# Kernel optimization log

Hardware: AMD Instinct MI355X
Metric: run time of the kernel (lower is better)

The kernel has to match this reference:

```python
import jax, jax.numpy as jnp
import numpy as np

IN_COUNT = 1024
OUT_COUNT = 1024
NUM_BASIS = 8
INPUT_ABS_MAX = 1.0
X_MIN = 0.0
X_MAX = 1.0
GAMMA_SCALE = 3.0
BATCH = 4096


def setup_inputs() -> dict:
    key = jax.random.key(0)
    k_x, k_c = jax.random.split(key)
    x = jax.random.normal(k_x, (BATCH, IN_COUNT), dtype=jnp.float32)
    coeffs = 0.01 * jax.random.normal(k_c, (OUT_COUNT, IN_COUNT, NUM_BASIS), dtype=jnp.float32)
    # fixed buffers
    centers_1d = jnp.linspace(X_MIN, X_MAX, NUM_BASIS)
    centers = jnp.broadcast_to(centers_1d[None, :], (IN_COUNT, NUM_BASIS)).astype(jnp.float32)
    delta = (X_MAX - X_MIN) / (NUM_BASIS - 1)
    gamma = GAMMA_SCALE / delta
    slopes = jnp.full((IN_COUNT, NUM_BASIS), gamma, dtype=jnp.float32)
    alpha = jnp.full((IN_COUNT,), (X_MAX - X_MIN) / (2.0 * INPUT_ABS_MAX), dtype=jnp.float32)
    beta = jnp.full((IN_COUNT,), 0.5 * (X_MIN + X_MAX), dtype=jnp.float32)
    return {"x": x, "coeffs": coeffs, "centers": centers, "slopes": slopes, "alpha": alpha, "beta": beta}


def reference(x, coeffs, centers, slopes, alpha, beta):
    # u: (B, in) affine transform with fixed alpha/beta
    u = alpha[None, :] * x + beta[None, :]
    # basis: (B, in, basis) = 0.5*(1+tanh(slope*(u - center)))
    basis = 0.5 * (1.0 + jnp.tanh(slopes[None, :, :] * (u[:, :, None] - centers[None, :, :])))
    # y[b,o] = sum_{i,m} coeffs[o,i,m] * basis[b,i,m]  (fused GEMM over in*basis)
    y = jnp.einsum('bim,oim->bo', basis, coeffs)
    return y
```

## Files before the change

kernel.cpp:

```cpp
#include <hip/hip_runtime.h>
#include <hip/hip_bf16.h>
#include <cstdint>
#include <cstddef>

#define BATCH 4096
#define INC   1024
#define OUTC  1024
#define NB    8
#define KDIM  (INC * NB)

#define BM 256
#define BN 256
#define BKB 64
#define SPLITS 4
#define KZ (KDIM / SPLITS)
#define KSTEPS (KZ / BKB)
#define GRID_BLOCKS ((OUTC / BN) * (BATCH / BM) * SPLITS)

#define EXPAND_BLOCKS  ((BATCH * INC) / 256)
#define QUANT_BLOCKS   OUTC
#define PREP_BLOCKS    (EXPAND_BLOCKS + QUANT_BLOCKS)

typedef int   v4i __attribute__((ext_vector_type(4)));
typedef char  v8c __attribute__((ext_vector_type(8)));
typedef short v8s __attribute__((ext_vector_type(8)));

__device__ __forceinline__ unsigned short f2bf(float f) {
  union { float f; unsigned u; } v; v.f = f;
  unsigned r = v.u + 0x7fffu + ((v.u >> 16) & 1u);
  return (unsigned short)(r >> 16);
}
__device__ __forceinline__ float bf2f(unsigned short h) {
  union { unsigned u; float f; } v; v.u = ((unsigned)h) << 16; return v.f;
}

__device__ __forceinline__ void gld16(const char* g, char* l) {
  __builtin_amdgcn_global_load_lds(
      (const __attribute__((address_space(1))) unsigned int*)g,
      (__attribute__((address_space(3))) unsigned int*)l, 16, 0, 0);
}

__global__ __launch_bounds__(256) void prep_kernel(
    const float* __restrict__ x, const float4* __restrict__ coeffs4,
    const float* __restrict__ centers, const float* __restrict__ slopes,
    const float* __restrict__ alpha, const float* __restrict__ beta,
    char* __restrict__ Ai8, int* __restrict__ Ci8i,
    float* __restrict__ maxrow, int* __restrict__ qcsum) {
  const int blk = blockIdx.x;
  const int tid = threadIdx.x;
  if (blk < EXPAND_BLOCKS) {
    const int idx = blk * 256 + tid;
    const int i = idx & (INC - 1);
    const float u = alpha[i] * x[idx] + beta[i];
    const float s0 = slopes[i * NB];
    const float c0 = centers[i * NB];
    const float c1 = centers[i * NB + 1];
    const float L2E2 = 2.8853900817779268f;
    const float a2 = L2E2 * s0;
    float e = __builtin_amdgcn_exp2f(a2 * (c0 - u));
    const float R = __builtin_amdgcn_exp2f(a2 * (c1 - c0));
    v8c q;
#pragma unroll
    for (int m = 0; m < 8; ++m) {
      float basis = __builtin_amdgcn_rcpf(1.0f + e);
      q[m] = (char)(int)rintf(basis * 254.0f - 127.0f);
      e *= R;
    }
    *(v8c*)(Ai8 + (size_t)idx * 8) = q;
  } else {
    const int o = blk - EXPAND_BLOCKS;
    const float4* row = coeffs4 + (size_t)o * (KDIM / 4);
    float4 v[8];
    float m = 0.0f;
#pragma unroll
    for (int j = 0; j < 8; ++j) {
      v[j] = row[tid + 256 * j];
      m = fmaxf(m, fmaxf(fmaxf(fabsf(v[j].x), fabsf(v[j].y)),
                         fmaxf(fabsf(v[j].z), fabsf(v[j].w))));
    }
#pragma unroll
    for (int off = 32; off; off >>= 1) m = fmaxf(m, __shfl_xor(m, off));
    __shared__ float wm[4];
    __shared__ int   wq[4];
    if ((tid & 63) == 0) wm[tid >> 6] = m;
    __syncthreads();
    const float M = fmaxf(fmaxf(fmaxf(wm[0], wm[1]), fmaxf(wm[2], wm[3])), 1e-30f);
    const float s = 127.0f / M;
    int qs = 0;
#pragma unroll
    for (int j = 0; j < 8; ++j) {
      int q0 = (int)rintf(v[j].x * s), q1 = (int)rintf(v[j].y * s);
      int q2 = (int)rintf(v[j].z * s), q3 = (int)rintf(v[j].w * s);
      Ci8i[(size_t)o * (KDIM / 4) + tid + 256 * j] =
          (q0 & 0xFF) | ((q1 & 0xFF) << 8) | ((q2 & 0xFF) << 16) | ((q3 & 0xFF) << 24);
      qs += q0 + q1 + q2 + q3;
    }
#pragma unroll
    for (int off = 32; off; off >>= 1) qs += __shfl_xor(qs, off);
    if ((tid & 63) == 0) wq[tid >> 6] = qs;
    __syncthreads();
    if (tid == 0) { maxrow[o] = M; qcsum[o] = wq[0] + wq[1] + wq[2] + wq[3]; }
  }
}

__global__ __launch_bounds__(512, 2) void gemm_kernel(
    const char* __restrict__ A, const char* __restrict__ C,
    unsigned short* __restrict__ partials) {
  __shared__ __align__(16) char As[3][BM * BKB];
  __shared__ __align__(16) char Bs[3][BN * BKB];

  const int id = (blockIdx.x & 7) * (GRID_BLOCKS / 8) + (blockIdx.x >> 3);
  const int z  = id >> 6;
  const int p  = id & 63;
  const int by = p >> 2;
  const int bx = p & 3;
  const int bm0 = by * BM;
  const int bn0 = bx * BN;
  const int kt0 = z * KZ;

  const int tid  = threadIdx.x;
  const int wave = tid >> 6;
  const int lane = tid & 63;
  const int quad = lane >> 4;
  const int lm   = lane & 15;
  const int wm   = (wave >> 2) * 128;
  const int wn   = (wave & 3) * 64;

  const int r4 = lane >> 2;
  const int gg = (lane & 3) ^ ((lane >> 3) & 3);

  const char* pA0 = A + (size_t)(bm0 + wave * 32 + r4) * KDIM + kt0 + gg * 16;
  const char* pB0 = C + (size_t)(bn0 + wave * 32 + r4) * KDIM + kt0 + gg * 16;
  const int lo = wave * 32 * BKB;

  v4i acc[8][4] = {};
  const int kx = (quad ^ ((lm >> 1) & 3)) * 16;

  static_assert(KSTEPS >= 3 && (KSTEPS - 2) % 1 == 0, "pipeline needs >=3 steps");

#define STAGE(SL)                                                            \
  {                                                                          \
    _Pragma("unroll")                                                        \
    for (int j = 0; j < 2; ++j) {                                            \
      gld16(pA0 + (size_t)j * (16 * KDIM), As[SL] + lo + j * (16 * BKB));    \
      gld16(pB0 + (size_t)j * (16 * KDIM), Bs[SL] + lo + j * (16 * BKB));    \
    }                                                                        \
    pA0 += BKB; pB0 += BKB;                                                  \
  }

#define STEP(SL, VMSTR, DOSTAGE)                                             \
  {                                                                          \
    asm volatile("s_waitcnt vmcnt(" VMSTR ")" ::: "memory");                 \
    __builtin_amdgcn_sched_barrier(0);                                       \
    __builtin_amdgcn_s_barrier();                                            \
    const char* cA = As[SL];                                                 \
    const char* cB = Bs[SL];                                                 \
    v4i a[4], b[4], a2[4];                                                   \
    _Pragma("unroll")                                                        \
    for (int f = 0; f < 4; ++f)                                              \
      a[f] = *(const v4i*)(cA + (wm + f * 16 + lm) * BKB + kx);              \
    _Pragma("unroll")                                                        \
    for (int f = 0; f < 4; ++f)                                              \
      b[f] = *(const v4i*)(cB + (wn + f * 16 + lm) * BKB + kx);              \
    _Pragma("unroll")                                                        \
    for (int f = 0; f < 4; ++f)                                              \
      a2[f] = *(const v4i*)(cA + (wm + (f + 4) * 16 + lm) * BKB + kx);       \
    asm volatile("s_waitcnt lgkmcnt(4)" ::: "memory");                       \
    __builtin_amdgcn_sched_barrier(0);                                       \
    __builtin_amdgcn_s_setprio(1);                                           \
    _Pragma("unroll")                                                        \
    for (int fm = 0; fm < 4; ++fm)                                           \
      _Pragma("unroll")                                                      \
      for (int fn = 0; fn < 4; ++fn)                                         \
        acc[fm][fn] = __builtin_amdgcn_mfma_i32_16x16x64_i8(a[fm], b[fn], acc[fm][fn], 0, 0, 0); \
    __builtin_amdgcn_s_setprio(0);                                           \
    asm volatile("s_waitcnt lgkmcnt(0)" ::: "memory");                       \
    __builtin_amdgcn_sched_barrier(0);                                       \
    __builtin_amdgcn_s_setprio(1);                                           \
    _Pragma("unroll")                                                        \
    for (int fm = 0; fm < 4; ++fm)                                           \
      _Pragma("unroll")                                                      \
      for (int fn = 0; fn < 4; ++fn)                                         \
        acc[fm + 4][fn] = __builtin_amdgcn_mfma_i32_16x16x64_i8(a2[fm], b[fn], acc[fm + 4][fn], 0, 0, 0); \
    __builtin_amdgcn_s_setprio(0);                                           \
    __builtin_amdgcn_s_barrier();                                            \
    if (DOSTAGE) STAGE(SL);                                                  \
  }

  STAGE(0);
  STAGE(1);
  STAGE(2);

  for (int t = 0; t < KSTEPS - 2; ++t) {
    const int sl = t % 3;
    STEP(sl, "8", (t < KSTEPS - 3));
  }
  STEP((KSTEPS - 2) % 3, "4", false);
  STEP((KSTEPS - 1) % 3, "0", false);
#undef STEP
#undef STAGE

  unsigned short* out = partials + (size_t)z * BATCH * OUTC;
#pragma unroll
  for (int fm = 0; fm < 8; ++fm) {
    const int row0 = bm0 + wm + fm * 16 + quad * 4;
#pragma unroll
    for (int fn = 0; fn < 4; ++fn) {
      const int col = bn0 + wn + fn * 16 + lm;
#pragma unroll
      for (int r = 0; r < 4; ++r)
        out[(size_t)(row0 + r) * OUTC + col] = f2bf((float)acc[fm][fn][r]);
    }
  }
}

__global__ __launch_bounds__(256) void reduce_kernel(
    const unsigned short* __restrict__ P, const float* __restrict__ maxrow,
    const int* __restrict__ qcsum, float* __restrict__ out) {
  const size_t nel = (size_t)BATCH * OUTC;
  const size_t base = ((size_t)blockIdx.x * 256 + threadIdx.x) * 8;
  float s[8] = {};
#pragma unroll
  for (int t = 0; t < SPLITS; ++t) {
    v8s v = *(const v8s*)(P + t * nel + base);
#pragma unroll
    for (int j = 0; j < 8; ++j) s[j] += bf2f((unsigned short)v[j]);
  }
  const int o0 = (int)(base & (OUTC - 1));
  const float inv = 1.0f / 32258.0f;
#pragma unroll
  for (int j = 0; j < 8; ++j) {
    const float M = maxrow[o0 + j];
    const int   Q = qcsum[o0 + j];
    s[j] = M * (s[j] + 127.0f * (float)Q) * inv;
  }
  *(float4*)(out + base)     = float4{s[0], s[1], s[2], s[3]};
  *(float4*)(out + base + 4) = float4{s[4], s[5], s[6], s[7]};
}

extern "C" void kernel_launch(void* const* d_in, const int* in_sizes, int n_in,
                              void* d_out, int out_size, void* d_ws, size_t ws_size,
                              hipStream_t stream) {
  const float* x       = (const float*)d_in[0];
  const float* coeffs  = (const float*)d_in[1];
  const float* centers = (const float*)d_in[2];
  const float* slopes  = (const float*)d_in[3];
  const float* alpha   = (const float*)d_in[4];
  const float* beta    = (const float*)d_in[5];
  float* out = (float*)d_out;

  const size_t a_bytes    = (size_t)BATCH * KDIM;
  const size_t c_bytes    = (size_t)OUTC * KDIM;
  const size_t stat_bytes = OUTC * sizeof(float);
  const size_t qcs_bytes  = OUTC * sizeof(int);
  const size_t part_bytes = (size_t)SPLITS * BATCH * OUTC * 2;
  if (ws_size < a_bytes + c_bytes + stat_bytes + qcs_bytes + part_bytes) return;

  char*  Ai8    = (char*)d_ws;
  char*  Ci8    = Ai8 + a_bytes;
  float* maxrow = (float*)(Ci8 + c_bytes);
  int*   qcsum  = (int*)((char*)maxrow + stat_bytes);
  unsigned short* parts = (unsigned short*)((char*)qcsum + qcs_bytes);

  prep_kernel<<<PREP_BLOCKS, 256, 0, stream>>>(
      x, (const float4*)coeffs, centers, slopes, alpha, beta,
      Ai8, (int*)Ci8, maxrow, qcsum);

  gemm_kernel<<<GRID_BLOCKS, 512, 0, stream>>>(Ai8, Ci8, parts);

  reduce_kernel<<<(int)((size_t)BATCH * OUTC / 8 / 256), 256, 0, stream>>>(
      parts, maxrow, qcsum, out);
}
```

Baseline: 160.2 us.

## Double-buffer LDS fragment registers to overlap reads with MFMA

```diff
diff --git a/kernel.cpp b/kernel.cpp
--- a/kernel.cpp
+++ b/kernel.cpp
@@ -133,72 +133,81 @@
   const char* pB0 = C + (size_t)(bn0 + wave * 32 + r4) * KDIM + kt0 + gg * 16;
   const int lo = wave * 32 * BKB;
 
+  const int kx   = (quad ^ ((lm >> 1) & 3)) * 16;
+  const int aoff = (wm + lm) * BKB + kx;
+  const int boff = (wn + lm) * BKB + kx;
+
   v4i acc[8][4] = {};
-  const int kx = (quad ^ ((lm >> 1) & 3)) * 16;
-
-  static_assert(KSTEPS >= 3 && (KSTEPS - 2) % 1 == 0, "pipeline needs >=3 steps");
-
-#define STAGE(SL)                                                            \
+  v4i a0v[8], b0v[4], a1v[8], b1v[4];
+  int srd = 0;
+  int sst = 0;
+
+#define STAGE_NEXT()                                                         \
   {                                                                          \
     _Pragma("unroll")                                                        \
     for (int j = 0; j < 2; ++j) {                                            \
-      gld16(pA0 + (size_t)j * (16 * KDIM), As[SL] + lo + j * (16 * BKB));    \
-      gld16(pB0 + (size_t)j * (16 * KDIM), Bs[SL] + lo + j * (16 * BKB));    \
+      gld16(pA0 + (size_t)j * (16 * KDIM), As[sst] + lo + j * (16 * BKB));   \
+      gld16(pB0 + (size_t)j * (16 * KDIM), Bs[sst] + lo + j * (16 * BKB));   \
     }                                                                        \
     pA0 += BKB; pB0 += BKB;                                                  \
-  }
-
-#define STEP(SL, VMSTR, DOSTAGE)                                             \
-  {                                                                          \
-    asm volatile("s_waitcnt vmcnt(" VMSTR ")" ::: "memory");                 \
+    sst = (sst == 2) ? 0 : sst + 1;                                          \
+  }
+
+#define READS(AV, BV)                                                        \
+  {                                                                          \
+    const char* cA = As[srd] + aoff;                                         \
+    const char* cB = Bs[srd] + boff;                                         \
+    _Pragma("unroll")                                                        \
+    for (int f = 0; f < 8; ++f) AV[f] = *(const v4i*)(cA + f * 16 * BKB);    \
+    _Pragma("unroll")                                                        \
+    for (int f = 0; f < 4; ++f) BV[f] = *(const v4i*)(cB + f * 16 * BKB);    \
+    srd = (srd == 2) ? 0 : srd + 1;                                          \
+  }
+
+#define MFMA32(AV, BV)                                                       \
+  {                                                                          \
+    __builtin_amdgcn_s_setprio(1);                                           \
+    _Pragma("unroll")                                                        \
+    for (int fm = 0; fm < 8; ++fm)                                           \
+      _Pragma("unroll")                                                      \
+      for (int fn = 0; fn < 4; ++fn)                                         \
+        acc[fm][fn] = __builtin_amdgcn_mfma_i32_16x16x64_i8(AV[fm], BV[fn], acc[fm][fn], 0, 0, 0); \
+    __builtin_amdgcn_s_setprio(0);                                           \
+  }
+
+#define STEP(CA, CB, NA, NBV, VMS, LGS, DOREADS, DOSTAGE)                    \
+  {                                                                          \
+    if (DOREADS) {                                                           \
+      asm volatile("s_waitcnt vmcnt(" VMS ")" ::: "memory");                 \
+      __builtin_amdgcn_sched_barrier(0);                                     \
+      __builtin_amdgcn_s_barrier();                                          \
+      READS(NA, NBV);                                                        \
+    }                                                                        \
+    asm volatile("s_waitcnt lgkmcnt(" LGS ")" ::: "memory");                 \
     __builtin_amdgcn_sched_barrier(0);                                       \
     __builtin_amdgcn_s_barrier();                                            \
-    const char* cA = As[SL];                                                 \
-    const char* cB = Bs[SL];                                                 \
-    v4i a[4], b[4], a2[4];                                                   \
-    _Pragma("unroll")                                                        \
-    for (int f = 0; f < 4; ++f)                                              \
-      a[f] = *(const v4i*)(cA + (wm + f * 16 + lm) * BKB + kx);              \
-    _Pragma("unroll")                                                        \
-    for (int f = 0; f < 4; ++f)                                              \
-      b[f] = *(const v4i*)(cB + (wn + f * 16 + lm) * BKB + kx);              \
-    _Pragma("unroll")                                                        \
-    for (int f = 0; f < 4; ++f)                                              \
-      a2[f] = *(const v4i*)(cA + (wm + (f + 4) * 16 + lm) * BKB + kx);       \
-    asm volatile("s_waitcnt lgkmcnt(4)" ::: "memory");                       \
-    __builtin_amdgcn_sched_barrier(0);                                       \
-    __builtin_amdgcn_s_setprio(1);                                           \
-    _Pragma("unroll")                                                        \
-    for (int fm = 0; fm < 4; ++fm)                                           \
-      _Pragma("unroll")                                                      \
-      for (int fn = 0; fn < 4; ++fn)                                         \
-        acc[fm][fn] = __builtin_amdgcn_mfma_i32_16x16x64_i8(a[fm], b[fn], acc[fm][fn], 0, 0, 0); \
-    __builtin_amdgcn_s_setprio(0);                                           \
-    asm volatile("s_waitcnt lgkmcnt(0)" ::: "memory");                       \
-    __builtin_amdgcn_sched_barrier(0);                                       \
-    __builtin_amdgcn_s_setprio(1);                                           \
-    _Pragma("unroll")                                                        \
-    for (int fm = 0; fm < 4; ++fm)                                           \
-      _Pragma("unroll")                                                      \
-      for (int fn = 0; fn < 4; ++fn)                                         \
-        acc[fm + 4][fn] = __builtin_amdgcn_mfma_i32_16x16x64_i8(a2[fm], b[fn], acc[fm + 4][fn], 0, 0, 0); \
-    __builtin_amdgcn_s_setprio(0);                                           \
-    __builtin_amdgcn_s_barrier();                                            \
-    if (DOSTAGE) STAGE(SL);                                                  \
-  }
-
-  STAGE(0);
-  STAGE(1);
-  STAGE(2);
-
-  for (int t = 0; t < KSTEPS - 2; ++t) {
-    const int sl = t % 3;
-    STEP(sl, "8", (t < KSTEPS - 3));
-  }
-  STEP((KSTEPS - 2) % 3, "4", false);
-  STEP((KSTEPS - 1) % 3, "0", false);
+    if (DOSTAGE) STAGE_NEXT();                                               \
+    MFMA32(CA, CB);                                                          \
+  }
+
+  STAGE_NEXT(); STAGE_NEXT(); STAGE_NEXT();
+  asm volatile("s_waitcnt vmcnt(8)" ::: "memory");
+  __builtin_amdgcn_sched_barrier(0);
+  __builtin_amdgcn_s_barrier();
+  READS(a0v, b0v);
+
+  for (int i = 0; i < 14; ++i) {
+    STEP(a0v, b0v, a1v, b1v, "4", "12", true, true);
+    STEP(a1v, b1v, a0v, b0v, "4", "12", true, true);
+  }
+  STEP(a0v, b0v, a1v, b1v, "4", "12", true, true);
+  STEP(a1v, b1v, a0v, b0v, "4", "12", true, false);
+  STEP(a0v, b0v, a1v, b1v, "0", "12", true, false);
+  STEP(a1v, b1v, a0v, b0v, "0", "0",  false, false);
 #undef STEP
-#undef STAGE
+#undef MFMA32
+#undef READS
+#undef STAGE_NEXT
 
   unsigned short* out = partials + (size_t)z * BATCH * OUTC;
 #pragma unroll
```

Result: faster. 152.8 us (-4.6%).
